# Performance work log

Measured on AMD Instinct MI355X. Metric: run time of the kernel, lower is better.

## Reference

```python
import jax, jax.numpy as jnp
import numpy as np

B, T = 8, 8192
D_X, D_H, D_K, D_V = 256, 512, 128, 128
RES_DIMS = [128, 128, 128, 128]
R = sum(RES_DIMS)
MEM_SLOTS, EP_TOPK = 256, 8
LN_EPS = 1e-5


def _ln(x, g, b):
    m = x.mean(-1, keepdims=True)
    v = ((x - m) ** 2).mean(-1, keepdims=True)
    return (x - m) * jax.lax.rsqrt(v + LN_EPS) * g + b


def _l2norm(x, eps=1e-8):
    return x / jnp.maximum(jnp.linalg.norm(x, axis=-1, keepdims=True), eps)


def setup_inputs() -> dict:
    key = jax.random.key(0)
    ks = jax.random.split(key, 12)
    def w(k, shape):  # xavier-ish scaling
        return jax.random.normal(k, shape, jnp.float32) * (shape[-1] ** -0.5)
    return dict(
        x_seq=jax.random.normal(ks[0], (B, T, D_X), jnp.float32),
        Wx_w=w(ks[1], (R, D_X)), Wx_b=jnp.zeros((R,), jnp.float32),
        Wh_w=w(ks[2], (R, D_H)),
        res_alpha=jnp.full((len(RES_DIMS),), -1.0, jnp.float32),
        A_scale=jnp.ones((D_H,), jnp.float32),
        B_w=w(ks[3], (D_H, R)),
        U_w=w(ks[4], (D_H, D_X)), U_b=jnp.zeros((D_H,), jnp.float32),
        fftn_g=jnp.ones((D_H,), jnp.float32), fftn_b=jnp.zeros((D_H,), jnp.float32),
        fftp_w=w(ks[5], (D_H, D_H)), fftp_b=jnp.zeros((D_H,), jnp.float32),
        fft_mix=jnp.asarray(0.5, jnp.float32),
        mix_logit=jnp.asarray(0.0, jnp.float32),
        key_w=w(ks[6], (D_K, R + D_X)), key_b=jnp.zeros((D_K,), jnp.float32),
        val_w=w(ks[7], (D_V, D_H)), val_b=jnp.zeros((D_V,), jnp.float32),
        rm_w=w(ks[8], (D_H, D_V)), rm_b=jnp.zeros((D_H,), jnp.float32),
        rn_g=jnp.ones((R,), jnp.float32), rn_b=jnp.zeros((R,), jnp.float32),
        mem_keys=jax.random.normal(ks[9], (B, MEM_SLOTS, D_K), jnp.float32),
        mem_vals=jax.random.normal(ks[10], (B, MEM_SLOTS, D_K), jnp.float32),
        heb_H=jax.random.normal(ks[11], (B, D_K, D_V), jnp.float32) * 0.1,
    )


def reference(x_seq, Wx_w, Wx_b, Wh_w, res_alpha, A_scale, B_w, U_w, U_b,
              fftn_g, fftn_b, fftp_w, fftp_b, fft_mix, mix_logit,
              key_w, key_b, val_w, val_b, rm_w, rm_b, rn_g, rn_b,
              mem_keys, mem_vals, heb_H):
    b = x_seq.shape[0]
    seg_index = np.repeat(np.arange(len(RES_DIMS)), RES_DIMS)  # static (R,)
    h_prev = jnp.zeros((b, D_H), x_seq.dtype)  # h0 = None
    r_prev = jnp.zeros((b, R), x_seq.dtype)    # r0 = None

    # reservoir update (fully parallel over T since h_prev/r_prev are broadcast)
    Wx = jnp.einsum('btx,rx->btr', x_seq, Wx_w) + Wx_b
    Wh = (h_prev @ Wh_w.T)[:, None, :]                    # (B,1,R), no bias in fwd
    alpha = jax.nn.sigmoid(res_alpha)[seg_index]          # (R,)
    r_seq = alpha * r_prev[:, None, :] + (1.0 - alpha) * jnp.tanh(Wx + Wh)
    r_seq = _ln(r_seq, rn_g, rn_b)

    # core state
    Ah = A_scale * h_prev[:, None, :]
    Bh = jnp.einsum('btr,hr->bth', r_seq, B_w)
    Uh = jnp.einsum('btx,hx->bth', x_seq, U_w) + U_b
    h_tilde = jax.nn.gelu(Ah + Bh + Uh, approximate=False)

    # FFT feature mixing
    h_norm = _ln(h_tilde, fftn_g, fftn_b)
    s = jax.nn.sigmoid(fft_mix)
    h_freq = jnp.fft.rfft(h_norm, n=D_H, axis=-1, norm='ortho')
    h_ifft = jnp.fft.irfft(h_freq * s, n=D_H, axis=-1, norm='ortho')
    h_fft_out = jnp.einsum('bth,oh->bto', h_ifft, fftp_w) + fftp_b
    hs = (1.0 - s) * h_tilde + s * h_fft_out

    # memory recall (once per sequence, batched)
    k = jnp.einsum('btf,kf->btk', jnp.concatenate([r_seq, x_seq], axis=-1), key_w) + key_b
    v = jnp.einsum('bth,vh->btv', hs, val_w) + val_b  # as in original (used for auto_write)
    c = _l2norm(k)
    q = c.mean(axis=1)                                # (B,d_k)

    # episodic: cosine top-k over slots, softmax-weighted value read
    kn = _l2norm(mem_keys)
    sim = jnp.einsum('bk,bmk->bm', _l2norm(q), kn)
    top_sim, top_idx = jax.lax.top_k(sim, EP_TOPK)
    w_att = jax.nn.softmax(top_sim, axis=-1)
    vals = jnp.take_along_axis(mem_vals, top_idx[..., None], axis=1)  # (B,topk,d_v)
    v_hat = jnp.einsum('bk,bkv->bv', w_att, vals)

    # hebbian: linear associative read from per-batch outer-product memory
    v_hebb = jnp.einsum('bk,bkv->bv', q, heb_H)

    mix = jax.nn.sigmoid(mix_logit)
    v_comb = mix * v_hat + (1.0 - mix) * v_hebb
    h_mem = v_comb @ rm_w.T + rm_b                    # (B,d_h)
    hs = hs + 0.5 * h_mem[:, None, :]
    return hs, r_seq
```

## Files before the change

### kernel.cpp

```cpp
#include <hip/hip_runtime.h>
#include <cmath>


typedef __attribute__((ext_vector_type(8)))  short short8;
typedef __attribute__((ext_vector_type(16))) float f32x16;

__device__ __forceinline__ unsigned short f2bf(float f) {
  union { float f; unsigned u; } v; v.f = f;
  unsigned r = v.u + 0x7FFF + ((v.u >> 16) & 1);
  return (unsigned short)(r >> 16);
}
__device__ __forceinline__ unsigned cvtpk(float lo, float hi) {
  unsigned r;
  asm("v_cvt_pk_bf16_f32 %0, %1, %2" : "=v"(r) : "v"(lo), "v"(hi));
  return r;
}
__device__ __forceinline__ float bf2f(unsigned short h) {
  union { unsigned u; float f; } v; v.u = ((unsigned)h) << 16; return v.f;
}
__device__ __forceinline__ f32x16 mfma16(short8 a, short8 b, f32x16 c) {
  return __builtin_amdgcn_mfma_f32_32x32x16_bf16(a, b, c, 0, 0, 0);
}
__device__ __forceinline__ void barrier_lgkm() {
  asm volatile("s_waitcnt lgkmcnt(0)" ::: "memory");
  __builtin_amdgcn_s_barrier();
  __builtin_amdgcn_sched_barrier(0);
}

__global__ __launch_bounds__(256) void k_wconv(
    const float* __restrict__ wx, const float* __restrict__ key,
    const float* __restrict__ bw, const float* __restrict__ uw,
    const float* __restrict__ fftpw, const float* __restrict__ fg,
    unsigned short* __restrict__ wxp, unsigned short* __restrict__ keyp,
    unsigned short* __restrict__ bwp, unsigned short* __restrict__ uwp,
    unsigned short* __restrict__ fftps) {
  int i = blockIdx.x * 256 + threadIdx.x;
  if (i >= 884736) return;
  float v; int n, k, N; unsigned short* dst;
  if (i < 131072)      { int j = i;          N = 512; k = j & 255; n = j >> 8; v = wx[j];  dst = wxp; }
  else if (i < 229376) { int j = i - 131072; N = 128; k = j % 768; n = j / 768; v = key[j]; dst = keyp; }
  else if (i < 491520) { int j = i - 229376; N = 512; k = j & 511; n = j >> 9; v = bw[j];  dst = bwp; }
  else if (i < 622592) { int j = i - 491520; N = 512; k = j & 255; n = j >> 8; v = uw[j];  dst = uwp; }
  else                 { int j = i - 622592; N = 512; k = j & 511; n = j >> 9; v = fftpw[j] * fg[k]; dst = fftps; }
  dst[(k >> 5) * (N * 32) + ((k >> 3) & 3) * (N * 8) + n * 8 + (k & 7)] = f2bf(v);
}

__global__ __launch_bounds__(512, 4) void k_rk(
    const float* __restrict__ x, const unsigned short* __restrict__ wxp,
    const unsigned short* __restrict__ keyp,
    const float* __restrict__ wxb, const float* __restrict__ resa,
    const float* __restrict__ rng, const float* __restrict__ rnb,
    const float* __restrict__ keyb,
    float* __restrict__ rout, float* __restrict__ partial) {
  __shared__ short sRX[24576];
  __shared__ float red[640];
  const int t = threadIdx.x, w = t >> 6, lane = t & 63, lr = lane & 31, lh = lane >> 5;
  const int m0 = blockIdx.x * 32;

#pragma unroll
  for (int i = 0; i < 4; ++i) {
    int c = t + i * 512;
    int row = c >> 6, k0 = (c & 63) * 4;
    float4 v = *reinterpret_cast<const float4*>(x + (size_t)(m0 + row) * 256 + k0);
    uint2 p;
    p.x = cvtpk(v.x, v.y);
    p.y = cvtpk(v.z, v.w);
    *reinterpret_cast<uint2*>(&sRX[16384 + (k0 >> 3) * 256 + row * 8 + (k0 & 7)]) = p;
  }
  barrier_lgkm();

  f32x16 acc[2];
#pragma unroll
  for (int ni = 0; ni < 2; ++ni)
#pragma unroll
    for (int e = 0; e < 16; ++e) acc[ni][e] = 0.f;
  short8 b0[4], b1[4];
  auto loadB0 = [&](int s, short8 (&bd)[4]) {
#pragma unroll
    for (int kh = 0; kh < 2; ++kh)
#pragma unroll
      for (int ni = 0; ni < 2; ++ni)
        bd[kh * 2 + ni] = *reinterpret_cast<const short8*>(
            wxp + (size_t)s * 16384 + (kh * 2 + lh) * 4096 + (64 * w + 32 * ni + lr) * 8);
  };
  auto mf0 = [&](int s, short8 (&bc)[4]) {
    short8 af[2];
#pragma unroll
    for (int kh = 0; kh < 2; ++kh)
      af[kh] = *reinterpret_cast<const short8*>(
          &sRX[16384 + (s * 4 + kh * 2 + lh) * 256 + lr * 8]);
    __builtin_amdgcn_s_setprio(1);
#pragma unroll
    for (int kh = 0; kh < 2; ++kh)
#pragma unroll
      for (int ni = 0; ni < 2; ++ni)
        acc[ni] = mfma16(af[kh], bc[kh * 2 + ni], acc[ni]);
    __builtin_amdgcn_s_setprio(0);
  };
  loadB0(0, b0);
#pragma unroll
  for (int s = 0; s < 8; s += 2) {
    loadB0(s + 1, b1);
    mf0(s, b0);
    if (s + 2 < 8) loadB0(s + 2, b0);
    mf0(s + 1, b1);
  }

#pragma unroll
  for (int ni = 0; ni < 2; ++ni) {
    int col = 64 * w + 32 * ni + lr;
    float al = 1.f / (1.f + expf(-resa[col >> 7]));
    float oma = 1.f - al, bbv = wxb[col];
#pragma unroll
    for (int r = 0; r < 16; ++r)
      acc[ni][r] = oma * tanhf(acc[ni][r] + bbv);
  }
#pragma unroll
  for (int r = 0; r < 16; ++r) {
    float s1 = acc[0][r] + acc[1][r];
    float s2 = acc[0][r] * acc[0][r] + acc[1][r] * acc[1][r];
#pragma unroll
    for (int m = 1; m <= 16; m <<= 1) { s1 += __shfl_xor(s1, m); s2 += __shfl_xor(s2, m); }
    int rl = (r & 3) + 8 * (r >> 2) + 4 * lh;
    if (lr == r) { red[w * 32 + rl] = s1; red[256 + w * 32 + rl] = s2; }
  }
  __syncthreads();
  if (t < 32) {
    float s1 = 0.f, s2 = 0.f;
#pragma unroll
    for (int n = 0; n < 8; ++n) { s1 += red[n * 32 + t]; s2 += red[256 + n * 32 + t]; }
    float mean = s1 * (1.f / 512.f);
    float var = s2 * (1.f / 512.f) - mean * mean;
    float rstd = rsqrtf(var + 1e-5f);
    red[512 + t * 2] = mean;
    red[512 + t * 2 + 1] = rstd;
  }
  __syncthreads();
#pragma unroll
  for (int q = 0; q < 4; ++q) {
    float4 stA = *reinterpret_cast<float4*>(&red[512 + (8 * q + 4 * lh) * 2]);
    float4 stB = *reinterpret_cast<float4*>(&red[512 + (8 * q + 4 * lh) * 2 + 4]);
    float mean[4] = {stA.x, stA.z, stB.x, stB.z};
    float rstd[4] = {stA.y, stA.w, stB.y, stB.w};
#pragma unroll
    for (int ni = 0; ni < 2; ++ni) {
      int col = 64 * w + 32 * ni + lr;
      float g = rng[col], bbv = rnb[col];
#pragma unroll
      for (int e = 0; e < 4; ++e) {
        int r = 4 * q + e;
        int rloc = 8 * q + 4 * lh + e;
        float val = (acc[ni][r] - mean[e]) * rstd[e] * g + bbv;
        rout[(size_t)(m0 + rloc) * 512 + col] = val;
        sRX[(col >> 3) * 256 + rloc * 8 + (col & 7)] = (short)f2bf(val);
      }
    }
  }
  barrier_lgkm();

  const int g = w >> 2, nw2 = w & 3;
  f32x16 ak;
#pragma unroll
  for (int e = 0; e < 16; ++e) ak[e] = 0.f;
  short8 kb0[2], kb1[2];
  auto loadBk = [&](int gc, short8 (&bd)[2]) {
#pragma unroll
    for (int kh = 0; kh < 2; ++kh)
      bd[kh] = *reinterpret_cast<const short8*>(
          keyp + (size_t)gc * 4096 + (kh * 2 + lh) * 1024 + (32 * nw2 + lr) * 8);
  };
  auto mfk = [&](int gc, short8 (&bc)[2]) {
    short8 af[2];
#pragma unroll
    for (int kh = 0; kh < 2; ++kh)
      af[kh] = *reinterpret_cast<const short8*>(
          &sRX[(gc * 4 + kh * 2 + lh) * 256 + lr * 8]);
    __builtin_amdgcn_s_setprio(1);
#pragma unroll
    for (int kh = 0; kh < 2; ++kh)
      ak = mfma16(af[kh], bc[kh], ak);
    __builtin_amdgcn_s_setprio(0);
  };
  const int gbase = g * 12;
  loadBk(gbase, kb0);
#pragma unroll
  for (int s = 0; s < 12; s += 2) {
    loadBk(gbase + s + 1, kb1);
    mfk(gbase + s, kb0);
    if (s + 2 < 12) loadBk(gbase + s + 2, kb0);
    mfk(gbase + s + 1, kb1);
  }
  __syncthreads();
  float* kp = reinterpret_cast<float*>(sRX);
#pragma unroll
  for (int r = 0; r < 16; ++r) {
    int rr = (r & 3) + 8 * (r >> 2) + 4 * lh;
    kp[g * 4096 + rr * 128 + nw2 * 32 + lr] = ak[r];
  }
  __syncthreads();
  {
    int rr = t >> 4, cg = t & 15;
    float s1 = 0.f;
#pragma unroll
    for (int j = 0; j < 8; ++j) {
      int c = cg * 8 + j;
      float v = kp[rr * 128 + c] + kp[4096 + rr * 128 + c] + keyb[c];
      s1 += v * v;
    }
#pragma unroll
    for (int m = 1; m <= 8; m <<= 1) s1 += __shfl_xor(s1, m);
    if (cg == 0) red[rr] = 1.f / fmaxf(sqrtf(s1), 1e-8f);
  }
  __syncthreads();
  if (t < 128) {
    float p = 0.f;
    float bb = keyb[t];
#pragma unroll 4
    for (int rr = 0; rr < 32; ++rr)
      p += (kp[rr * 128 + t] + kp[4096 + rr * 128 + t] + bb) * red[rr];
    partial[(size_t)blockIdx.x * 128 + t] = p;
  }
}

__global__ __launch_bounds__(256) void k_qred(const float* __restrict__ partial,
                                              float* __restrict__ q_ws) {
  int gid = blockIdx.x * 256 + threadIdx.x;
  int b = gid >> 7, c = gid & 127;
  float s = 0.f;
  for (int i = 0; i < 256; ++i) s += partial[(size_t)(b * 256 + i) * 128 + c];
  q_ws[gid] = s * (1.f / 8192.f);
}

__global__ __launch_bounds__(256) void k_cvec(const float* __restrict__ fb,
                                              const float* __restrict__ fftpw,
                                              float* __restrict__ cvec) {
  int o = blockIdx.x * 256 + threadIdx.x;
  const float* w = fftpw + (size_t)o * 512;
  float s = 0.f;
  for (int k = 0; k < 512; ++k) s += fb[k] * w[k];
  cvec[o] = s;
}

__global__ __launch_bounds__(256) void k_mem(
    const float* __restrict__ q_ws, const float* __restrict__ mkeys,
    const float* __restrict__ mvals, const float* __restrict__ hebH,
    const float* __restrict__ rmw, const float* __restrict__ rmb,
    const float* __restrict__ mixl, float* __restrict__ hm) {
  const int b = blockIdx.x, t = threadIdx.x;
  __shared__ float qv[128];
  __shared__ float ssim[256];
  __shared__ float red[256];
  __shared__ float tval[8];
  __shared__ int tidx[8];
  __shared__ float wsm[8];
  __shared__ float vcs[128];

  if (t < 128) qv[t] = q_ws[b * 128 + t];
  __syncthreads();
  red[t] = (t < 128) ? qv[t] * qv[t] : 0.f;
  __syncthreads();
  for (int s = 128; s > 0; s >>= 1) {
    if (t < s) red[t] += red[t + s];
    __syncthreads();
  }
  float qsc = 1.f / fmaxf(sqrtf(red[0]), 1e-8f);
  {
    const float* mk = mkeys + ((size_t)b * 256 + t) * 128;
    float dot = 0.f, ms = 0.f;
    for (int k = 0; k < 128; ++k) { float mv = mk[k]; dot += qv[k] * mv; ms += mv * mv; }
    ssim[t] = dot * qsc / fmaxf(sqrtf(ms), 1e-8f);
  }
  __syncthreads();
  for (int it = 0; it < 8; ++it) {
    if (t < 64) {
      float bv = -1e30f; int bi = 0;
#pragma unroll
      for (int u = 0; u < 4; ++u) {
        int m = t * 4 + u;
        float v = ssim[m];
        if (v > bv) { bv = v; bi = m; }
      }
      for (int off = 32; off; off >>= 1) {
        float ov = __shfl_xor(bv, off, 64);
        int oi = __shfl_xor(bi, off, 64);
        if (ov > bv || (ov == bv && oi < bi)) { bv = ov; bi = oi; }
      }
      if (t == 0) { tval[it] = bv; tidx[it] = bi; ssim[bi] = -1e30f; }
    }
    __syncthreads();
  }
  if (t == 0) {
    float m0 = tval[0], sum = 0.f, e[8];
#pragma unroll
    for (int i = 0; i < 8; ++i) { e[i] = expf(tval[i] - m0); sum += e[i]; }
#pragma unroll
    for (int i = 0; i < 8; ++i) wsm[i] = e[i] / sum;
  }
  __syncthreads();
  float mix = 1.f / (1.f + expf(-mixl[0]));
  if (t < 128) {
    float vh = 0.f;
#pragma unroll
    for (int i = 0; i < 8; ++i) vh += wsm[i] * mvals[((size_t)b * 256 + tidx[i]) * 128 + t];
    float vhb = 0.f;
    const float* H = hebH + (size_t)b * 128 * 128;
    for (int k = 0; k < 128; ++k) vhb += qv[k] * H[k * 128 + t];
    vcs[t] = mix * vh + (1.f - mix) * vhb;
  }
  __syncthreads();
  for (int h = t; h < 512; h += 256) {
    float sum = rmb[h];
    const float* wr = rmw + (size_t)h * 128;
    for (int v = 0; v < 128; ++v) sum += vcs[v] * wr[v];
    hm[b * 512 + h] = sum;
  }
}

__global__ __launch_bounds__(512, 4) void k_fused(
    const float* __restrict__ rseq, const float* __restrict__ x,
    const unsigned short* __restrict__ buw,
    const float* __restrict__ ub, const unsigned short* __restrict__ fftps,
    const float* __restrict__ fftpb, const float* __restrict__ fmix,
    const float* __restrict__ cvec, const float* __restrict__ hm,
    float* __restrict__ hs) {
  __shared__ short sRX[24576];
  __shared__ float red[640];
  const int t = threadIdx.x, w = t >> 6, lane = t & 63, lr = lane & 31, lh = lane >> 5;
  const int m0 = blockIdx.x * 32;
  const int bidx = m0 >> 13;

#pragma unroll
  for (int i = 0; i < 8; ++i) {
    int c = t + i * 512;
    int row = c >> 7, k0 = (c & 127) * 4;
    float4 v = *reinterpret_cast<const float4*>(rseq + (size_t)(m0 + row) * 512 + k0);
    uint2 p;
    p.x = cvtpk(v.x, v.y);
    p.y = cvtpk(v.z, v.w);
    *reinterpret_cast<uint2*>(&sRX[(k0 >> 3) * 256 + row * 8 + (k0 & 7)]) = p;
  }
#pragma unroll
  for (int i = 0; i < 4; ++i) {
    int c = t + i * 512;
    int row = c >> 6, k0 = (c & 63) * 4;
    float4 v = *reinterpret_cast<const float4*>(x + (size_t)(m0 + row) * 256 + k0);
    uint2 p;
    p.x = cvtpk(v.x, v.y);
    p.y = cvtpk(v.z, v.w);
    *reinterpret_cast<uint2*>(&sRX[16384 + (k0 >> 3) * 256 + row * 8 + (k0 & 7)]) = p;
  }
  barrier_lgkm();

  f32x16 acc[2];
#pragma unroll
  for (int ni = 0; ni < 2; ++ni)
#pragma unroll
    for (int e = 0; e < 16; ++e) acc[ni][e] = 0.f;
  short8 b0[4], b1[4];
  auto loadB1 = [&](int s, short8 (&bd)[4]) {
#pragma unroll
    for (int kh = 0; kh < 2; ++kh)
#pragma unroll
      for (int ni = 0; ni < 2; ++ni)
        bd[kh * 2 + ni] = *reinterpret_cast<const short8*>(
            buw + (size_t)s * 16384 + (kh * 2 + lh) * 4096 + (64 * w + 32 * ni + lr) * 8);
  };
  auto mf1 = [&](int s, short8 (&bc)[4]) {
    short8 af[2];
#pragma unroll
    for (int kh = 0; kh < 2; ++kh)
      af[kh] = *reinterpret_cast<const short8*>(
          &sRX[(s * 4 + kh * 2 + lh) * 256 + lr * 8]);
    __builtin_amdgcn_s_setprio(1);
#pragma unroll
    for (int kh = 0; kh < 2; ++kh)
#pragma unroll
      for (int ni = 0; ni < 2; ++ni)
        acc[ni] = mfma16(af[kh], bc[kh * 2 + ni], acc[ni]);
    __builtin_amdgcn_s_setprio(0);
  };
  loadB1(0, b0);
#pragma unroll
  for (int s = 0; s < 24; s += 2) {
    loadB1(s + 1, b1);
    mf1(s, b0);
    if (s + 2 < 24) loadB1(s + 2, b0);
    mf1(s + 1, b1);
  }

#pragma unroll
  for (int ni = 0; ni < 2; ++ni) {
    int col = 64 * w + 32 * ni + lr;
    float ubc = ub[col];
#pragma unroll
    for (int r = 0; r < 16; ++r) {
      float pre = acc[ni][r] + ubc;
      acc[ni][r] = 0.5f * pre * (1.f + erff(pre * 0.70710678118654752f));
    }
  }
#pragma unroll
  for (int r = 0; r < 16; ++r) {
    float s1 = acc[0][r] + acc[1][r];
    float s2 = acc[0][r] * acc[0][r] + acc[1][r] * acc[1][r];
#pragma unroll
    for (int m = 1; m <= 16; m <<= 1) { s1 += __shfl_xor(s1, m); s2 += __shfl_xor(s2, m); }
    int rl = (r & 3) + 8 * (r >> 2) + 4 * lh;
    if (lr == r) { red[w * 32 + rl] = s1; red[256 + w * 32 + rl] = s2; }
  }
  __syncthreads();
  if (t < 32) {
    float s1 = 0.f, s2 = 0.f;
#pragma unroll
    for (int n = 0; n < 8; ++n) { s1 += red[n * 32 + t]; s2 += red[256 + n * 32 + t]; }
    float mean = s1 * (1.f / 512.f);
    float var = s2 * (1.f / 512.f) - mean * mean;
    float rstd = rsqrtf(var + 1e-5f);
    red[512 + t * 2] = mean;
    red[512 + t * 2 + 1] = rstd;
  }
  __syncthreads();
  unsigned htp[2][8];
#pragma unroll
  for (int ni = 0; ni < 2; ++ni)
#pragma unroll
    for (int p = 0; p < 8; ++p)
      htp[ni][p] = cvtpk(acc[ni][2 * p], acc[ni][2 * p + 1]);
  auto loadB2 = [&](int s, short8 (&bd)[4]) {
#pragma unroll
    for (int kh = 0; kh < 2; ++kh)
#pragma unroll
      for (int ni = 0; ni < 2; ++ni)
        bd[kh * 2 + ni] = *reinterpret_cast<const short8*>(
            fftps + (size_t)s * 16384 + (kh * 2 + lh) * 4096 + (64 * w + 32 * ni + lr) * 8);
  };
  loadB2(0, b0);
#pragma unroll
  for (int q = 0; q < 4; ++q) {
    float4 stA = *reinterpret_cast<float4*>(&red[512 + (8 * q + 4 * lh) * 2]);
    float4 stB = *reinterpret_cast<float4*>(&red[512 + (8 * q + 4 * lh) * 2 + 4]);
    float mean[4] = {stA.x, stA.z, stB.x, stB.z};
    float rstd[4] = {stA.y, stA.w, stB.y, stB.w};
#pragma unroll
    for (int ni = 0; ni < 2; ++ni) {
      int col = 64 * w + 32 * ni + lr;
#pragma unroll
      for (int e = 0; e < 4; ++e) {
        int r = 4 * q + e;
        float z = (acc[ni][r] - mean[e]) * rstd[e];
        int rloc = 8 * q + 4 * lh + e;
        sRX[(col >> 3) * 256 + rloc * 8 + (col & 7)] = (short)f2bf(z);
      }
    }
  }
#pragma unroll
  for (int ni = 0; ni < 2; ++ni)
#pragma unroll
    for (int e = 0; e < 16; ++e) acc[ni][e] = 0.f;
  barrier_lgkm();

  auto mf2 = [&](int s, short8 (&bc)[4]) {
    short8 af[2];
#pragma unroll
    for (int kh = 0; kh < 2; ++kh)
      af[kh] = *reinterpret_cast<const short8*>(
          &sRX[(s * 4 + kh * 2 + lh) * 256 + lr * 8]);
    __builtin_amdgcn_s_setprio(1);
#pragma unroll
    for (int kh = 0; kh < 2; ++kh)
#pragma unroll
      for (int ni = 0; ni < 2; ++ni)
        acc[ni] = mfma16(af[kh], bc[kh * 2 + ni], acc[ni]);
    __builtin_amdgcn_s_setprio(0);
  };
#pragma unroll
  for (int s = 0; s < 16; s += 2) {
    loadB2(s + 1, b1);
    mf2(s, b0);
    if (s + 2 < 16) loadB2(s + 2, b0);
    mf2(s + 1, b1);
  }

  const float sg = 1.f / (1.f + expf(-fmix[0]));
  const float s2f = sg * sg, oms = 1.f - sg;
#pragma unroll
  for (int ni = 0; ni < 2; ++ni) {
    int col = 64 * w + 32 * ni + lr;
    float base = s2f * cvec[col] + sg * fftpb[col] + 0.5f * hm[bidx * 512 + col];
#pragma unroll
    for (int p = 0; p < 8; ++p) {
      unsigned pk = htp[ni][p];
      int r0 = 2 * p;
      int rloc = (r0 & 3) + 8 * (r0 >> 2) + 4 * lh;
      float o0 = oms * bf2f((unsigned short)(pk & 0xFFFF)) + s2f * acc[ni][r0] + base;
      float o1 = oms * bf2f((unsigned short)(pk >> 16)) + s2f * acc[ni][r0 + 1] + base;
      hs[(size_t)(m0 + rloc) * 512 + col] = o0;
      hs[(size_t)(m0 + rloc + 1) * 512 + col] = o1;
    }
  }
}

extern "C" void kernel_launch(void* const* d_in, const int* in_sizes, int n_in,
                              void* d_out, int out_size, void* d_ws, size_t ws_size,
                              hipStream_t stream) {
  (void)in_sizes; (void)n_in; (void)out_size; (void)ws_size;
  const float* x     = (const float*)d_in[0];
  const float* Wxw   = (const float*)d_in[1];
  const float* Wxb   = (const float*)d_in[2];
  const float* resa  = (const float*)d_in[4];
  const float* Bw    = (const float*)d_in[6];
  const float* Uw    = (const float*)d_in[7];
  const float* Ub    = (const float*)d_in[8];
  const float* fg    = (const float*)d_in[9];
  const float* fb    = (const float*)d_in[10];
  const float* fftpw = (const float*)d_in[11];
  const float* fftpb = (const float*)d_in[12];
  const float* fmix  = (const float*)d_in[13];
  const float* mixl  = (const float*)d_in[14];
  const float* keyw  = (const float*)d_in[15];
  const float* keyb  = (const float*)d_in[16];
  const float* rmw   = (const float*)d_in[19];
  const float* rmb   = (const float*)d_in[20];
  const float* rng   = (const float*)d_in[21];
  const float* rnb   = (const float*)d_in[22];
  const float* mkeys = (const float*)d_in[23];
  const float* mvals = (const float*)d_in[24];
  const float* hebH  = (const float*)d_in[25];

  float* outp = (float*)d_out;
  float* hs   = outp;
  float* rout = outp + (size_t)65536 * 512;

  unsigned short* wsu = (unsigned short*)d_ws;
  unsigned short* wxp    = wsu;
  unsigned short* keyp   = wsu + 131072;
  unsigned short* bwp    = wsu + 229376;
  unsigned short* uwp    = wsu + 491520;
  unsigned short* fftps  = wsu + 622592;
  float* wsf     = (float*)d_ws;
  float* partial = wsf + 524288;
  float* q_ws    = wsf + 786432;
  float* hm      = wsf + 787456;
  float* cvec    = wsf + 791552;

  k_wconv<<<3456, 256, 0, stream>>>(Wxw, keyw, Bw, Uw, fftpw, fg,
                                    wxp, keyp, bwp, uwp, fftps);
  k_cvec <<<2,    256, 0, stream>>>(fb, fftpw, cvec);
  k_rk   <<<2048, 512, 0, stream>>>(x, wxp, keyp, Wxb, resa, rng, rnb, keyb,
                                    rout, partial);
  k_qred <<<4,    256, 0, stream>>>(partial, q_ws);
  k_mem  <<<8,    256, 0, stream>>>(q_ws, mkeys, mvals, hebH, rmw, rmb, mixl, hm);
  k_fused<<<2048, 512, 0, stream>>>(rout, x, bwp, Ub, fftps, fftpb,
                                    fmix, cvec, hm, hs);
}
```

Baseline: 306.6 us.

## Cut register pressure in fused kernel to raise occupancy bound

Raises the launch-bounds occupancy hint from 4 to 6 waves per SIMD and halves the register-resident B-fragment prefetch buffers by stepping the MFMA loops over half-K-steps. It also drops the packed bf16 copy of the GELU output held in registers across the second GEMM; the epilogue instead reconstructs h_tilde from the normalized bf16 values already in shared memory, using a stored sqrt(var+eps) and the mean. This frees registers for higher occupancy, at the cost of shallower prefetch, extra LDS reads, and an extra rounding step: h_tilde is rebuilt from bf16 normalized values rather than directly from the activations.

```diff
diff --git a/kernel.cpp b/kernel.cpp
--- a/kernel.cpp
+++ b/kernel.cpp
@@ -316,7 +316,7 @@
   }
 }
 
-__global__ __launch_bounds__(512, 4) void k_fused(
+__global__ __launch_bounds__(512, 6) void k_fused(
     const float* __restrict__ rseq, const float* __restrict__ x,
     const unsigned short* __restrict__ buw,
     const float* __restrict__ ub, const unsigned short* __restrict__ fftps,
@@ -356,36 +356,30 @@
   for (int ni = 0; ni < 2; ++ni)
 #pragma unroll
     for (int e = 0; e < 16; ++e) acc[ni][e] = 0.f;
-  short8 b0[4], b1[4];
-  auto loadB1 = [&](int s, short8 (&bd)[4]) {
-#pragma unroll
-    for (int kh = 0; kh < 2; ++kh)
-#pragma unroll
-      for (int ni = 0; ni < 2; ++ni)
-        bd[kh * 2 + ni] = *reinterpret_cast<const short8*>(
-            buw + (size_t)s * 16384 + (kh * 2 + lh) * 4096 + (64 * w + 32 * ni + lr) * 8);
-  };
-  auto mf1 = [&](int s, short8 (&bc)[4]) {
-    short8 af[2];
-#pragma unroll
-    for (int kh = 0; kh < 2; ++kh)
-      af[kh] = *reinterpret_cast<const short8*>(
-          &sRX[(s * 4 + kh * 2 + lh) * 256 + lr * 8]);
+  short8 b0[2], b1[2];
+  auto loadB1 = [&](int h, short8 (&bd)[2]) {
+#pragma unroll
+    for (int ni = 0; ni < 2; ++ni)
+      bd[ni] = *reinterpret_cast<const short8*>(
+          buw + (size_t)(h >> 1) * 16384 + ((h & 1) * 2 + lh) * 4096 +
+          (64 * w + 32 * ni + lr) * 8);
+  };
+  auto mf1 = [&](int h, short8 (&bc)[2]) {
+    short8 af = *reinterpret_cast<const short8*>(
+        &sRX[(h * 2 + lh) * 256 + lr * 8]);
     __builtin_amdgcn_s_setprio(1);
 #pragma unroll
-    for (int kh = 0; kh < 2; ++kh)
-#pragma unroll
-      for (int ni = 0; ni < 2; ++ni)
-        acc[ni] = mfma16(af[kh], bc[kh * 2 + ni], acc[ni]);
+    for (int ni = 0; ni < 2; ++ni)
+      acc[ni] = mfma16(af, bc[ni], acc[ni]);
     __builtin_amdgcn_s_setprio(0);
   };
   loadB1(0, b0);
 #pragma unroll
-  for (int s = 0; s < 24; s += 2) {
-    loadB1(s + 1, b1);
-    mf1(s, b0);
-    if (s + 2 < 24) loadB1(s + 2, b0);
-    mf1(s + 1, b1);
+  for (int h = 0; h < 48; h += 2) {
+    loadB1(h + 1, b1);
+    mf1(h, b0);
+    if (h + 2 < 48) loadB1(h + 2, b0);
+    mf1(h + 1, b1);
   }
 
 #pragma unroll
@@ -417,21 +411,15 @@
     float rstd = rsqrtf(var + 1e-5f);
     red[512 + t * 2] = mean;
     red[512 + t * 2 + 1] = rstd;
-  }
-  __syncthreads();
-  unsigned htp[2][8];
-#pragma unroll
-  for (int ni = 0; ni < 2; ++ni)
-#pragma unroll
-    for (int p = 0; p < 8; ++p)
-      htp[ni][p] = cvtpk(acc[ni][2 * p], acc[ni][2 * p + 1]);
-  auto loadB2 = [&](int s, short8 (&bd)[4]) {
-#pragma unroll
-    for (int kh = 0; kh < 2; ++kh)
-#pragma unroll
-      for (int ni = 0; ni < 2; ++ni)
-        bd[kh * 2 + ni] = *reinterpret_cast<const short8*>(
-            fftps + (size_t)s * 16384 + (kh * 2 + lh) * 4096 + (64 * w + 32 * ni + lr) * 8);
+    red[576 + t] = sqrtf(var + 1e-5f);
+  }
+  __syncthreads();
+  auto loadB2 = [&](int h, short8 (&bd)[2]) {
+#pragma unroll
+    for (int ni = 0; ni < 2; ++ni)
+      bd[ni] = *reinterpret_cast<const short8*>(
+          fftps + (size_t)(h >> 1) * 16384 + ((h & 1) * 2 + lh) * 4096 +
+          (64 * w + 32 * ni + lr) * 8);
   };
   loadB2(0, b0);
 #pragma unroll
@@ -458,26 +446,21 @@
     for (int e = 0; e < 16; ++e) acc[ni][e] = 0.f;
   barrier_lgkm();
 
-  auto mf2 = [&](int s, short8 (&bc)[4]) {
-    short8 af[2];
-#pragma unroll
-    for (int kh = 0; kh < 2; ++kh)
-      af[kh] = *reinterpret_cast<const short8*>(
-          &sRX[(s * 4 + kh * 2 + lh) * 256 + lr * 8]);
+  auto mf2 = [&](int h, short8 (&bc)[2]) {
+    short8 af = *reinterpret_cast<const short8*>(
+        &sRX[(h * 2 + lh) * 256 + lr * 8]);
     __builtin_amdgcn_s_setprio(1);
 #pragma unroll
-    for (int kh = 0; kh < 2; ++kh)
-#pragma unroll
-      for (int ni = 0; ni < 2; ++ni)
-        acc[ni] = mfma16(af[kh], bc[kh * 2 + ni], acc[ni]);
+    for (int ni = 0; ni < 2; ++ni)
+      acc[ni] = mfma16(af, bc[ni], acc[ni]);
     __builtin_amdgcn_s_setprio(0);
   };
 #pragma unroll
-  for (int s = 0; s < 16; s += 2) {
-    loadB2(s + 1, b1);
-    mf2(s, b0);
-    if (s + 2 < 16) loadB2(s + 2, b0);
-    mf2(s + 1, b1);
+  for (int h = 0; h < 32; h += 2) {
+    loadB2(h + 1, b1);
+    mf2(h, b0);
+    if (h + 2 < 32) loadB2(h + 2, b0);
+    mf2(h + 1, b1);
   }
 
   const float sg = 1.f / (1.f + expf(-fmix[0]));
@@ -486,16 +469,17 @@
   for (int ni = 0; ni < 2; ++ni) {
     int col = 64 * w + 32 * ni + lr;
     float base = s2f * cvec[col] + sg * fftpb[col] + 0.5f * hm[bidx * 512 + col];
-#pragma unroll
-    for (int p = 0; p < 8; ++p) {
-      unsigned pk = htp[ni][p];
-      int r0 = 2 * p;
-      int rloc = (r0 & 3) + 8 * (r0 >> 2) + 4 * lh;
-      float o0 = oms * bf2f((unsigned short)(pk & 0xFFFF)) + s2f * acc[ni][r0] + base;
-      float o1 = oms * bf2f((unsigned short)(pk >> 16)) + s2f * acc[ni][r0 + 1] + base;
-      hs[(size_t)(m0 + rloc) * 512 + col] = o0;
-      hs[(size_t)(m0 + rloc + 1) * 512 + col] = o1;
-    }
+    const int cb = (col >> 3) * 256 + (col & 7);
+#pragma unroll
+    for (int q = 0; q < 4; ++q)
+#pragma unroll
+      for (int e = 0; e < 4; ++e) {
+        int r = 4 * q + e;
+        int rloc = 8 * q + 4 * lh + e;
+        float z = bf2f((unsigned short)sRX[cb + rloc * 8]);
+        float ht = z * red[576 + rloc] + red[512 + rloc * 2];
+        hs[(size_t)(m0 + rloc) * 512 + col] = oms * ht + s2f * acc[ni][r] + base;
+      }
   }
 }
 
```

Result: slower. 401.5 us (+30.9%).
